# Performance work log

Hardware: AMD Instinct MI355X
Metric: run time of the kernel (lower is better)

## Reference

```python
import jax, jax.numpy as jnp
import numpy as np

B, S, D, H = 4, 2048, 1024, 16
HD = D // H  # 64


def setup_inputs() -> dict:
    key = jax.random.key(0)
    ks = jax.random.split(key, 11)
    scale = 1.0 / np.sqrt(D)
    inp = {
        "query": jax.random.normal(ks[0], (B, S, D), jnp.float32),
        "key": jax.random.normal(ks[1], (B, S, D), jnp.float32),
        "value": jax.random.normal(ks[2], (B, S, D), jnp.float32),
        "mask": jnp.ones((B, 1, 1, S), jnp.float32),
        "wq": jax.random.normal(ks[3], (D, D), jnp.float32) * scale,
        "bq": jnp.zeros((D,), jnp.float32),
        "wk": jax.random.normal(ks[4], (D, D), jnp.float32) * scale,
        "bk": jnp.zeros((D,), jnp.float32),
        "wv": jax.random.normal(ks[5], (D, D), jnp.float32) * scale,
        "bv": jnp.zeros((D,), jnp.float32),
        "wo": jax.random.normal(ks[6], (D, D), jnp.float32) * scale,
        "bo": jnp.zeros((D,), jnp.float32),
    }
    return inp


def reference(query, key, value, mask, wq, bq, wk, bk, wv, bv, wo, bo):
    b = query.shape[0]
    # Dense QKV projections
    q = query @ wq + bq  # [B,S,D]
    k = key @ wk + bk
    v = value @ wv + bv

    def split_heads(x):
        return x.reshape(b, -1, H, HD).transpose(0, 2, 1, 3)  # [B,H,S,HD]

    q, k, v = split_heads(q), split_heads(k), split_heads(v)
    score = jnp.einsum("bhqd,bhkd->bhqk", q, k) / jnp.sqrt(jnp.float32(HD))
    score = score + (1.0 - mask) * -1e9
    alpha = jax.nn.softmax(score, axis=-1)
    context = jnp.einsum("bhqk,bhkd->bhqd", alpha, v)  # [B,H,S,HD]
    context = context.transpose(0, 2, 1, 3).reshape(b, -1, D)
    return context @ wo + bo
```

## Files before the change

### kernel.cpp

```cpp
#include <hip/hip_runtime.h>

using u16 = unsigned short;
using u32 = unsigned int;

typedef float  f32x4  __attribute__((ext_vector_type(4)));
typedef float  f32x16 __attribute__((ext_vector_type(16)));
typedef u32    u32x4  __attribute__((ext_vector_type(4)));
typedef _Float16 f16;
typedef f16 f16x8 __attribute__((ext_vector_type(8)));

#define DEVI static __device__ __forceinline__

constexpr int S_  = 2048;
constexpr int D_  = 1024;
constexpr int HD_ = 64;
constexpr int SH_ = S_*HD_;
constexpr size_t NE_ = 8192ull*1024ull;

DEVI f32x4 mfma16f(f16x8 a, f16x8 b, f32x4 c){
  return __builtin_amdgcn_mfma_f32_16x16x32_f16(a, b, c, 0, 0, 0);
}
DEVI f32x16 mfma32(f16x8 a, f16x8 b, f32x16 c){
  return __builtin_amdgcn_mfma_f32_32x32x16_f16(a, b, c, 0, 0, 0);
}
DEVI float exp2fast(float x){
#if __has_builtin(__builtin_amdgcn_exp2f)
  return __builtin_amdgcn_exp2f(x);
#else
  float r; asm("v_exp_f32 %0, %1" : "=v"(r) : "v"(x)); return r;
#endif
}
DEVI float rcpfast(float x){
#if __has_builtin(__builtin_amdgcn_rcpf)
  return __builtin_amdgcn_rcpf(x);
#else
  float r; asm("v_rcp_f32 %0, %1" : "=v"(r) : "v"(x)); return r;
#endif
}
DEVI u32 pkh(float a, float b){
  return __builtin_bit_cast(u32, __builtin_amdgcn_cvt_pkrtz(a, b));
}
DEVI void gld16(const void* g, void* l){
  __builtin_amdgcn_global_load_lds(
      (const __attribute__((address_space(1))) u32*)g,
      (__attribute__((address_space(3))) u32*)l, 16, 0, 0);
}
DEVI void gld4(const void* g, void* l){
  __builtin_amdgcn_global_load_lds(
      (const __attribute__((address_space(1))) u32*)g,
      (__attribute__((address_space(3))) u32*)l, 4, 0, 0);
}

__global__ __launch_bounds__(256) void wcvt_k(
    const float* __restrict__ wq, const float* __restrict__ wk,
    const float* __restrict__ wv, const float* __restrict__ wo,
    u16* __restrict__ wt)
{
  int z = blockIdx.z;
  const float* W = (z==0)?wq:(z==1)?wk:(z==2)?wv:wo;
  u16* ot = wt + (size_t)z*D_*D_;
  __shared__ float t[64][65];
  int k0 = blockIdx.y*64, n0 = blockIdx.x*64;
  int tid = threadIdx.x;
#pragma unroll
  for (int i=0;i<4;i++){
    int lin = i*256 + tid;
    int r = lin>>4, c = (lin&15)*4;
    f32x4 v = *reinterpret_cast<const f32x4*>(W + (size_t)(k0+r)*D_ + n0 + c);
    t[r][c+0]=v.x; t[r][c+1]=v.y; t[r][c+2]=v.z; t[r][c+3]=v.w;
  }
  __syncthreads();
  int n = tid>>2, c0 = (tid&3)*16;
  alignas(16) u16 hb[16];
#pragma unroll
  for (int i=0;i<16;i++) hb[i] = __builtin_bit_cast(u16, (f16)t[c0+i][n]);
  size_t off = (size_t)(n0+n)*D_ + k0 + c0;
  *reinterpret_cast<u32x4*>(ot+off)   = *reinterpret_cast<u32x4*>(hb);
  *reinterpret_cast<u32x4*>(ot+off+8) = *reinterpret_cast<u32x4*>(hb+8);
}

__global__ __launch_bounds__(256) void madd_k(const float* __restrict__ mask,
                                              float* __restrict__ madd2)
{
  int i = blockIdx.x*256 + threadIdx.x;
  if (i < 4*S_) madd2[i] = (1.0f - mask[i]) * -1442695040.0f;
}

struct GemmArgs {
  const void* A[3];
  const u16*  Wt[3];
  const float* bias[3];
  float*      outF[3];
  u16*        outH[3];
  float       scale[3];
  int         mode[3];
};

template<bool AF32>
__global__ __launch_bounds__(512, 4) void gemm_k(GemmArgs args)
{
  int z = blockIdx.z;
  const float* __restrict__ Af   = (const float*)args.A[z];
  const u16*   __restrict__ Ah   = (const u16*)args.A[z];
  const u16*   __restrict__ Wt   = args.Wt[z];
  const float* __restrict__ bias = args.bias[z];
  int mode = args.mode[z];
  float sc = args.scale[z];

  constexpr int ABYT = 16384;
  constexpr int BUFS = ABYT + 8192;
  __shared__ __align__(16) unsigned char smem[73728];
  char* sbase = (char*)smem;

  int m0 = blockIdx.x*256, n0 = blockIdx.y*128;
  int tid = threadIdx.x, lane = tid&63, w = tid>>6;
  int wm = (w>>1)*64, wn = (w&1)*64;
  int lr = lane&15, lh = lane>>4;

  int offA[2], offB;
#pragma unroll
  for (int j=0;j<2;j++){
    int chunk = w*2 + j;
    int row = chunk*16 + (lane>>2);
    int gs = lane&3;
    offA[j] = row*D_ + (((gs - (row>>1)) & 3)*8);
  }
  {
    int row = w*16 + (lane>>2);
    int gs = lane&3;
    offB = row*D_ + (((gs - (row>>1)) & 3)*8);
  }

  int arow = w*32 + (lane>>1);
  const float* Abase = AF32 ? (Af + (size_t)(m0 + arow)*D_ + (lane&1)*16)
                            : (const float*)nullptr;

  f32x4 acc[4][4];
#pragma unroll
  for (int m=0;m<4;m++)
#pragma unroll
    for (int n=0;n<4;n++) acc[m][n] = f32x4{0.f,0.f,0.f,0.f};

  auto BSTAGE = [&](int kt){
    char* lB = sbase + (kt - (kt/3)*3)*BUFS + ABYT;
    gld16(Wt + (size_t)n0*D_ + kt*32 + offB, lB + w*1024);
  };
  auto ASTAGE16 = [&](int kt){
    char* lA = sbase + (kt - (kt/3)*3)*BUFS;
    const u16* As = Ah + (size_t)m0*D_ + kt*32;
#pragma unroll
    for (int j=0;j<2;j++) gld16(As + offA[j], lA + (w*2+j)*1024);
  };

  f32x4 ra0, ra1, ra2, ra3;

#define AISSUE_M(kt) { \
  ra0 = *reinterpret_cast<const f32x4*>(Abase + (kt)*32 + 0); \
  ra1 = *reinterpret_cast<const f32x4*>(Abase + (kt)*32 + 4); \
  ra2 = *reinterpret_cast<const f32x4*>(Abase + (kt)*32 + 8); \
  ra3 = *reinterpret_cast<const f32x4*>(Abase + (kt)*32 + 12); }

#define CONVERT_M(bufA) { \
  u32x4 w0_, w1_; \
  w0_.x = pkh(ra0.x,ra0.y); w0_.y = pkh(ra0.z,ra0.w); \
  w0_.z = pkh(ra1.x,ra1.y); w0_.w = pkh(ra1.z,ra1.w); \
  w1_.x = pkh(ra2.x,ra2.y); w1_.y = pkh(ra2.z,ra2.w); \
  w1_.z = pkh(ra3.x,ra3.y); w1_.w = pkh(ra3.z,ra3.w); \
  char* dst_ = (bufA) + arow*64; \
  int g0_ = (lane&1)*2; \
  *reinterpret_cast<u32x4*>(dst_ + (((g0_   + (arow>>1))&3)<<4)) = w0_; \
  *reinterpret_cast<u32x4*>(dst_ + (((g0_+1 + (arow>>1))&3)<<4)) = w1_; }

  if constexpr (AF32){
    BSTAGE(0); BSTAGE(1); BSTAGE(2);
    AISSUE_M(0);
    CONVERT_M(sbase);
    AISSUE_M(1);
    asm volatile("s_waitcnt vmcnt(6)" ::: "memory");

    for (int t=0; t<32; ++t){
      int buf = t - (t/3)*3;
      char* bA = sbase + buf*BUFS;
      char* bB = bA + ABYT;

      asm volatile("s_waitcnt lgkmcnt(0)" ::: "memory");
      __builtin_amdgcn_s_barrier();
      __builtin_amdgcn_sched_barrier(0);

      f16x8 af[4], bfr[4];
#pragma unroll
      for (int m=0;m<4;m++){
        int row = wm + m*16 + lr;
        af[m] = *reinterpret_cast<const f16x8*>(bA + row*64 + (((lh + (row>>1)) & 3)<<4));
      }
#pragma unroll
      for (int n=0;n<4;n++){
        int row = wn + n*16 + lr;
        bfr[n] = *reinterpret_cast<const f16x8*>(bB + row*64 + (((lh + (row>>1)) & 3)<<4));
      }
      asm volatile("s_waitcnt lgkmcnt(0)" ::: "memory");
      __builtin_amdgcn_sched_barrier(0);
      __builtin_amdgcn_s_barrier();

      if (t < 31){
        asm volatile("s_waitcnt vmcnt(0)" ::: "memory");
        int nb = (t+1) - ((t+1)/3)*3;
        CONVERT_M(sbase + nb*BUFS);
      }
      if (t < 30) AISSUE_M(t+2);
      if (t < 29) BSTAGE(t+3);

      __builtin_amdgcn_s_setprio(1);
#pragma unroll
      for (int m=0;m<4;m++)
#pragma unroll
        for (int n=0;n<4;n++)
          acc[m][n] = mfma16f(af[m], bfr[n], acc[m][n]);
      __builtin_amdgcn_s_setprio(0);
    }
  } else {
    ASTAGE16(0); BSTAGE(0);
    ASTAGE16(1); BSTAGE(1);
    ASTAGE16(2); BSTAGE(2);

    for (int t=0; t<32; ++t){
      int buf = t - (t/3)*3;
      if (t < 30)       asm volatile("s_waitcnt vmcnt(6)" ::: "memory");
      else if (t == 30) asm volatile("s_waitcnt vmcnt(3)" ::: "memory");
      else              asm volatile("s_waitcnt vmcnt(0)" ::: "memory");
      __builtin_amdgcn_s_barrier();

      char* bA = sbase + buf*BUFS;
      char* bB = bA + ABYT;
      f16x8 af[4], bfr[4];
#pragma unroll
      for (int m=0;m<4;m++){
        int row = wm + m*16 + lr;
        af[m] = *reinterpret_cast<const f16x8*>(bA + row*64 + (((lh + (row>>1)) & 3)<<4));
      }
#pragma unroll
      for (int n=0;n<4;n++){
        int row = wn + n*16 + lr;
        bfr[n] = *reinterpret_cast<const f16x8*>(bB + row*64 + (((lh + (row>>1)) & 3)<<4));
      }
      asm volatile("s_waitcnt lgkmcnt(0)" ::: "memory");
      __builtin_amdgcn_sched_barrier(0);
      __builtin_amdgcn_s_barrier();
      if (t < 29){ ASTAGE16(t+3); BSTAGE(t+3); }

      __builtin_amdgcn_s_setprio(1);
#pragma unroll
      for (int m=0;m<4;m++)
#pragma unroll
        for (int n=0;n<4;n++)
          acc[m][n] = mfma16f(af[m], bfr[n], acc[m][n]);
      __builtin_amdgcn_s_setprio(0);
    }
  }
#undef AISSUE_M
#undef CONVERT_M

  float bsetv[4];
#pragma unroll
  for (int n=0;n<4;n++) bsetv[n] = bias[n0 + wn + n*16 + lr];

  if (mode == 0){
    float* out = args.outF[z];
#pragma unroll
    for (int m=0;m<4;m++)
#pragma unroll
      for (int n=0;n<4;n++)
#pragma unroll
        for (int r=0;r<4;r++){
          int row = m0 + wm + m*16 + lh*4 + r;
          int col = n0 + wn + n*16 + lr;
          out[(size_t)row*D_ + col] = (acc[m][n][r] + bsetv[n])*sc;
        }
  } else if (mode == 1){
    u16* oh = args.outH[z];
#pragma unroll
    for (int m=0;m<4;m++)
#pragma unroll
      for (int n=0;n<4;n++)
#pragma unroll
        for (int r=0;r<4;r++){
          int row = m0 + wm + m*16 + lh*4 + r;
          int col = n0 + wn + n*16 + lr;
          float val = (acc[m][n][r] + bsetv[n])*sc;
          int b = row >> 11, s = row & 2047;
          int hh = col >> 6,  dd = col & 63;
          oh[(size_t)(b*16 + hh)*SH_ + (size_t)s*HD_ + dd] =
              __builtin_bit_cast(u16, (f16)val);
        }
  } else {
    __syncthreads();
    u16* ct = (u16*)sbase;
#pragma unroll
    for (int m=0;m<4;m++)
#pragma unroll
      for (int n=0;n<4;n++)
#pragma unroll
        for (int r=0;r<4;r++){
          int lrow = wm + m*16 + lh*4 + r;
          int lcol = wn + n*16 + lr;
          ct[lrow*132 + lcol] = __builtin_bit_cast(u16, (f16)((acc[m][n][r] + bsetv[n])*sc));
        }
    __syncthreads();
    u16* ovt = args.outH[z];
    int b = m0 >> 11, s0 = m0 & 2047;
    int ch = tid >> 2, quarter = tid & 3;
    int gn = n0 + ch;
    int hh = gn >> 6, dd = gn & 63;
    size_t obase = (size_t)(b*16 + hh)*SH_ + (size_t)dd*S_ + s0 + quarter*64;
#pragma unroll
    for (int i=0;i<8;i++){
      alignas(16) u16 tmp[8];
#pragma unroll
      for (int j=0;j<8;j++) tmp[j] = ct[(quarter*64 + i*8 + j)*132 + ch];
      *reinterpret_cast<u32x4*>(ovt + obase + i*8) = *reinterpret_cast<u32x4*>(tmp);
    }
  }
}

__global__ __launch_bounds__(256, 2) void attn_k(
    const f16* __restrict__ Qf, const f16* __restrict__ Kf,
    const f16* __restrict__ Vt, const float* __restrict__ madd2,
    u16* __restrict__ cf)
{
  constexpr int BUFS = 33280;
  __shared__ __align__(16) unsigned char smem[2*BUFS];
  char* sbase = (char*)smem;

  int flat = blockIdx.x + blockIdx.y*gridDim.x;
  int xcd = flat & 7, ix = flat >> 3;
  int bh = xcd + 8*(ix >> 4);
  int qx = ix & 15;
  int b = bh >> 4, head = bh & 15;

  const f16* Qb = Qf + (size_t)bh*SH_;
  const f16* Kb = Kf + (size_t)bh*SH_;
  const f16* Vb = Vt + (size_t)bh*SH_;
  const float* mb = madd2 + (size_t)b*S_;

  int tid = threadIdx.x, lane = tid&63, w = tid>>6;
  int q31 = lane&31, h = lane>>5;
  int qw = qx*128 + w*32;
  int xorv = (q31&7)<<4;

  f16x8 qb[4];
#pragma unroll
  for (int ks=0;ks<4;ks++)
    qb[ks] = *reinterpret_cast<const f16x8*>(Qb + (size_t)(qw + q31)*HD_ + ks*16 + h*8);

  int offK[4], offV[4];
#pragma unroll
  for (int j=0;j<4;j++){
    int L = (w*4+j)*1024 + lane*16;
    int rK = L>>7;
    int dbyK = (L&127) ^ ((rK&7)<<4);
    offK[j] = rK*HD_ + (dbyK>>1);
    int rV = L>>8;
    int dbyV = (L&255) ^ ((rV&7)<<4);
    offV[j] = rV*S_ + (dbyV>>1);
  }

  u32 one2 = 0x3C003C00u;
  u32x4 onev; onev.x=one2; onev.y=one2; onev.z=one2; onev.w=one2;
  f16x8 vones = __builtin_bit_cast(f16x8, onev);

  f32x16 z16;
#pragma unroll
  for (int r=0;r<16;r++) z16[r] = 0.f;

  f32x16 o[2], ol;
#pragma unroll
  for (int n=0;n<2;n++)
#pragma unroll
    for (int r=0;r<16;r++) o[n][r] = 0.f;
#pragma unroll
  for (int r=0;r<16;r++) ol[r] = 0.f;

  auto STAGE = [&](int buf, int t){
    int kv0 = t*128;
    char* sKb = sbase + buf*BUFS;
    char* sVb = sKb + 16384;
    char* sMb = sKb + 32768;
#pragma unroll
    for (int j=0;j<4;j++)
      gld16(Kb + (size_t)kv0*HD_ + offK[j], sKb + (w*4+j)*1024);
#pragma unroll
    for (int j=0;j<4;j++)
      gld16(Vb + kv0 + offV[j], sVb + (w*4+j)*1024);
    gld4(mb + kv0 + lane, sMb);
    gld4(mb + kv0 + 64 + lane, sMb + 256);
  };

  STAGE(0, 0);
  STAGE(1, 1);

  for (int t=0; t<16; ++t){
    int buf = t&1;
    char* sKb = sbase + buf*BUFS;
    char* sVb = sKb + 16384;
    float* sMb = (float*)(sKb + 32768);

    if (t < 15) asm volatile("s_waitcnt vmcnt(10)" ::: "memory");
    else        asm volatile("s_waitcnt vmcnt(0)"  ::: "memory");
    __builtin_amdgcn_s_barrier();
    __builtin_amdgcn_sched_barrier(0);

    f32x16 stA[2], stB[2];

    __builtin_amdgcn_s_setprio(1);
#pragma unroll
    for (int n=0;n<2;n++){
      int rb = (n*32 + q31)*128;
      f16x8 ka = *reinterpret_cast<const f16x8*>(sKb + ((rb + h*16) ^ xorv));
      stA[n] = mfma32(ka, qb[0], z16);
#pragma unroll
      for (int ks=1;ks<4;ks++){
        ka = *reinterpret_cast<const f16x8*>(sKb + ((rb + ks*32 + h*16) ^ xorv));
        stA[n] = mfma32(ka, qb[ks], stA[n]);
      }
    }
#pragma unroll
    for (int n=0;n<2;n++){
      int rb = (64 + n*32 + q31)*128;
      f16x8 ka = *reinterpret_cast<const f16x8*>(sKb + ((rb + h*16) ^ xorv));
      stB[n] = mfma32(ka, qb[0], z16);
#pragma unroll
      for (int ks=1;ks<4;ks++){
        ka = *reinterpret_cast<const f16x8*>(sKb + ((rb + ks*32 + h*16) ^ xorv));
        stB[n] = mfma32(ka, qb[ks], stB[n]);
      }
    }
    __builtin_amdgcn_s_setprio(0);

    auto SMPV = [&](int sub, f32x16 (&st)[2]){
      float mval = sMb[sub*64 + lane];
      if (__ballot(mval != 0.0f)){
#pragma unroll
        for (int n=0;n<2;n++)
#pragma unroll
          for (int g=0;g<4;g++){
            f32x4 mv = *reinterpret_cast<const f32x4*>(sMb + sub*64 + n*32 + g*8 + h*4);
#pragma unroll
            for (int c=0;c<4;c++) st[n][g*4+c] += mv[c];
          }
      }
#pragma unroll
      for (int n=0;n<2;n++)
#pragma unroll
        for (int r=0;r<16;r++) st[n][r] = exp2fast(st[n][r]);

      f16x8 pa[4];
#pragma unroll
      for (int n=0;n<2;n++){
        u32 x[4], y[4];
#pragma unroll
        for (int T=0;T<4;T++){
          x[T] = pkh(st[n][4*T+0], st[n][4*T+1]);
          y[T] = pkh(st[n][4*T+2], st[n][4*T+3]);
        }
#pragma unroll
        for (int k2=0;k2<2;k2++){
          u32 a0=x[2*k2], b0=x[2*k2+1], a1=y[2*k2], b1=y[2*k2+1];
          asm volatile("v_permlane32_swap_b32 %0, %1" : "+v"(a0), "+v"(b0));
          asm volatile("v_permlane32_swap_b32 %0, %1" : "+v"(a1), "+v"(b1));
          u32x4 wv;
          wv.x = a0;
          wv.y = a1;
          wv.z = b0;
          wv.w = b1;
          pa[2*n+k2] = __builtin_bit_cast(f16x8, wv);
        }
      }

      __builtin_amdgcn_s_setprio(1);
#pragma unroll
      for (int n=0;n<2;n++){
        int rbv = (n*32 + q31)*256 + sub*128;
#pragma unroll
        for (int ks=0;ks<4;ks++){
          f16x8 vbf = *reinterpret_cast<const f16x8*>(sVb + ((rbv + ks*32 + h*16) ^ xorv));
          o[n] = mfma32(pa[ks], vbf, o[n]);
        }
      }
#pragma unroll
      for (int ks=0;ks<4;ks++)
        ol = mfma32(pa[ks], vones, ol);
      __builtin_amdgcn_s_setprio(0);
    };

    SMPV(0, stA);
    SMPV(1, stB);

    asm volatile("s_waitcnt lgkmcnt(0)" ::: "memory");
    __builtin_amdgcn_s_barrier();
    __builtin_amdgcn_sched_barrier(0);
    if (t < 14) STAGE(buf, t+2);
  }

#pragma unroll
  for (int n=0;n<2;n++)
#pragma unroll
    for (int r=0;r<16;r++){
      float inv = rcpfast(ol[r]);
      int s = qw + (r&3) + 8*(r>>2) + 4*h;
      int d = head*HD_ + n*32 + q31;
      cf[((size_t)(b*S_ + s))*D_ + d] = __builtin_bit_cast(u16, (f16)(o[n][r]*inv));
    }
}

extern "C" void kernel_launch(void* const* d_in, const int* in_sizes, int n_in,
                              void* d_out, int out_size, void* d_ws, size_t ws_size,
                              hipStream_t stream)
{
  (void)in_sizes; (void)n_in; (void)out_size;
  const float* query=(const float*)d_in[0];
  const float* key  =(const float*)d_in[1];
  const float* value=(const float*)d_in[2];
  const float* mask =(const float*)d_in[3];
  const float* wq=(const float*)d_in[4];
  const float* bq=(const float*)d_in[5];
  const float* wk=(const float*)d_in[6];
  const float* bk=(const float*)d_in[7];
  const float* wv=(const float*)d_in[8];
  const float* bv=(const float*)d_in[9];
  const float* wo=(const float*)d_in[10];
  const float* bo=(const float*)d_in[11];
  float* out = (float*)d_out;

  const size_t WN = 4ull*1024*1024;
  size_t need = WN*2 + 4*NE_*2 + 8192*4;
  if (ws_size < need) return;

  char* ws = (char*)d_ws;
  u16* wt = (u16*)ws;
  u16* qf = wt + WN;
  u16* kf = qf + NE_;
  u16* vt = kf + NE_;
  u16* cf = vt + NE_;
  float* madd2 = (float*)(cf + NE_);

  const float CSC = 0.18033688011112042f;

  wcvt_k<<<dim3(16,16,4), 256, 0, stream>>>(wq,wk,wv,wo,wt);
  madd_k<<<dim3(32), 256, 0, stream>>>(mask, madd2);

  GemmArgs ga{};
  ga.A[0]=query; ga.A[1]=key; ga.A[2]=value;
  ga.Wt[0]=wt;           ga.Wt[1]=wt+1048576;   ga.Wt[2]=wt+2097152;
  ga.bias[0]=bq; ga.bias[1]=bk; ga.bias[2]=bv;
  ga.scale[0]=CSC; ga.scale[1]=1.0f; ga.scale[2]=1.0f;
  ga.mode[0]=1;  ga.mode[1]=1;  ga.mode[2]=2;
  ga.outH[0]=qf; ga.outH[1]=kf; ga.outH[2]=vt;
  gemm_k<true><<<dim3(32,8,3), 512, 0, stream>>>(ga);

  attn_k<<<dim3(16,64), 256, 0, stream>>>((const f16*)qf,(const f16*)kf,(const f16*)vt,madd2,cf);

  GemmArgs go{};
  go.A[0]=cf;
  go.Wt[0]=wt+3145728;
  go.bias[0]=bo; go.scale[0]=1.0f; go.mode[0]=0; go.outF[0]=out;
  gemm_k<false><<<dim3(32,8,1), 512, 0, stream>>>(go);
}
```

Baseline: 205.0 us.

## Double-buffer fp32 A register prefetch to deepen GEMM load pipeline

```diff
diff --git a/kernel.cpp b/kernel.cpp
--- a/kernel.cpp
+++ b/kernel.cpp
@@ -152,71 +152,86 @@
     for (int j=0;j<2;j++) gld16(As + offA[j], lA + (w*2+j)*1024);
   };
 
-  f32x4 ra0, ra1, ra2, ra3;
-
-#define AISSUE_M(kt) { \
-  ra0 = *reinterpret_cast<const f32x4*>(Abase + (kt)*32 + 0); \
-  ra1 = *reinterpret_cast<const f32x4*>(Abase + (kt)*32 + 4); \
-  ra2 = *reinterpret_cast<const f32x4*>(Abase + (kt)*32 + 8); \
-  ra3 = *reinterpret_cast<const f32x4*>(Abase + (kt)*32 + 12); }
-
-#define CONVERT_M(bufA) { \
+  f32x4 s0a, s0b, s0c, s0d;
+  f32x4 s1a, s1b, s1c, s1d;
+
+#define AISSUE0(kt) { \
+  s0a = *reinterpret_cast<const f32x4*>(Abase + (kt)*32 + 0); \
+  s0b = *reinterpret_cast<const f32x4*>(Abase + (kt)*32 + 4); \
+  s0c = *reinterpret_cast<const f32x4*>(Abase + (kt)*32 + 8); \
+  s0d = *reinterpret_cast<const f32x4*>(Abase + (kt)*32 + 12); }
+#define AISSUE1(kt) { \
+  s1a = *reinterpret_cast<const f32x4*>(Abase + (kt)*32 + 0); \
+  s1b = *reinterpret_cast<const f32x4*>(Abase + (kt)*32 + 4); \
+  s1c = *reinterpret_cast<const f32x4*>(Abase + (kt)*32 + 8); \
+  s1d = *reinterpret_cast<const f32x4*>(Abase + (kt)*32 + 12); }
+
+#define CONVERT_GEN(pa,pb,pc,pd,bufA) { \
   u32x4 w0_, w1_; \
-  w0_.x = pkh(ra0.x,ra0.y); w0_.y = pkh(ra0.z,ra0.w); \
-  w0_.z = pkh(ra1.x,ra1.y); w0_.w = pkh(ra1.z,ra1.w); \
-  w1_.x = pkh(ra2.x,ra2.y); w1_.y = pkh(ra2.z,ra2.w); \
-  w1_.z = pkh(ra3.x,ra3.y); w1_.w = pkh(ra3.z,ra3.w); \
+  w0_.x = pkh(pa.x,pa.y); w0_.y = pkh(pa.z,pa.w); \
+  w0_.z = pkh(pb.x,pb.y); w0_.w = pkh(pb.z,pb.w); \
+  w1_.x = pkh(pc.x,pc.y); w1_.y = pkh(pc.z,pc.w); \
+  w1_.z = pkh(pd.x,pd.y); w1_.w = pkh(pd.z,pd.w); \
   char* dst_ = (bufA) + arow*64; \
   int g0_ = (lane&1)*2; \
   *reinterpret_cast<u32x4*>(dst_ + (((g0_   + (arow>>1))&3)<<4)) = w0_; \
   *reinterpret_cast<u32x4*>(dst_ + (((g0_+1 + (arow>>1))&3)<<4)) = w1_; }
+#define CONVERT0(bufA) CONVERT_GEN(s0a,s0b,s0c,s0d,bufA)
+#define CONVERT1(bufA) CONVERT_GEN(s1a,s1b,s1c,s1d,bufA)
+
+#define AF32_BODY(t, CVTSET) { \
+  int buf_ = (t) - ((t)/3)*3; \
+  char* bA_ = sbase + buf_*BUFS; \
+  char* bB_ = bA_ + ABYT; \
+  if ((t) < 30)      asm volatile("s_waitcnt vmcnt(10)" ::: "memory"); \
+  else if ((t)==30)  asm volatile("s_waitcnt vmcnt(5)"  ::: "memory"); \
+  else               asm volatile("s_waitcnt vmcnt(0)"  ::: "memory"); \
+  asm volatile("s_waitcnt lgkmcnt(0)" ::: "memory"); \
+  __builtin_amdgcn_s_barrier(); \
+  __builtin_amdgcn_sched_barrier(0); \
+  f16x8 af_[4], bf_[4]; \
+  _Pragma("unroll") \
+  for (int m=0;m<4;m++){ \
+    int row = wm + m*16 + lr; \
+    af_[m] = *reinterpret_cast<const f16x8*>(bA_ + row*64 + (((lh + (row>>1)) & 3)<<4)); \
+  } \
+  _Pragma("unroll") \
+  for (int n=0;n<4;n++){ \
+    int row = wn + n*16 + lr; \
+    bf_[n] = *reinterpret_cast<const f16x8*>(bB_ + row*64 + (((lh + (row>>1)) & 3)<<4)); \
+  } \
+  asm volatile("s_waitcnt lgkmcnt(0)" ::: "memory"); \
+  __builtin_amdgcn_sched_barrier(0); \
+  __builtin_amdgcn_s_barrier(); \
+  if ((t) < 31){ \
+    int nb_ = ((t)+1) - (((t)+1)/3)*3; \
+    if constexpr (CVTSET == 0) { CONVERT0(sbase + nb_*BUFS); } \
+    else                       { CONVERT1(sbase + nb_*BUFS); } \
+  } \
+  if ((t) < 29){ \
+    if constexpr (CVTSET == 0) { AISSUE0((t)+3); } \
+    else                       { AISSUE1((t)+3); } \
+    BSTAGE((t)+3); \
+  } \
+  __builtin_amdgcn_s_setprio(1); \
+  _Pragma("unroll") \
+  for (int m=0;m<4;m++) \
+    _Pragma("unroll") \
+    for (int n=0;n<4;n++) \
+      acc[m][n] = mfma16f(af_[m], bf_[n], acc[m][n]); \
+  __builtin_amdgcn_s_setprio(0); }
 
   if constexpr (AF32){
     BSTAGE(0); BSTAGE(1); BSTAGE(2);
-    AISSUE_M(0);
-    CONVERT_M(sbase);
-    AISSUE_M(1);
-    asm volatile("s_waitcnt vmcnt(6)" ::: "memory");
-
-    for (int t=0; t<32; ++t){
-      int buf = t - (t/3)*3;
-      char* bA = sbase + buf*BUFS;
-      char* bB = bA + ABYT;
-
-      asm volatile("s_waitcnt lgkmcnt(0)" ::: "memory");
-      __builtin_amdgcn_s_barrier();
-      __builtin_amdgcn_sched_barrier(0);
-
-      f16x8 af[4], bfr[4];
-#pragma unroll
-      for (int m=0;m<4;m++){
-        int row = wm + m*16 + lr;
-        af[m] = *reinterpret_cast<const f16x8*>(bA + row*64 + (((lh + (row>>1)) & 3)<<4));
-      }
-#pragma unroll
-      for (int n=0;n<4;n++){
-        int row = wn + n*16 + lr;
-        bfr[n] = *reinterpret_cast<const f16x8*>(bB + row*64 + (((lh + (row>>1)) & 3)<<4));
-      }
-      asm volatile("s_waitcnt lgkmcnt(0)" ::: "memory");
-      __builtin_amdgcn_sched_barrier(0);
-      __builtin_amdgcn_s_barrier();
-
-      if (t < 31){
-        asm volatile("s_waitcnt vmcnt(0)" ::: "memory");
-        int nb = (t+1) - ((t+1)/3)*3;
-        CONVERT_M(sbase + nb*BUFS);
-      }
-      if (t < 30) AISSUE_M(t+2);
-      if (t < 29) BSTAGE(t+3);
-
-      __builtin_amdgcn_s_setprio(1);
-#pragma unroll
-      for (int m=0;m<4;m++)
-#pragma unroll
-        for (int n=0;n<4;n++)
-          acc[m][n] = mfma16f(af[m], bfr[n], acc[m][n]);
-      __builtin_amdgcn_s_setprio(0);
+    AISSUE0(0);
+    CONVERT0(sbase);
+    AISSUE1(1);
+    AISSUE0(2);
+
+    for (int i=0; i<16; ++i){
+      int u = 2*i, v = 2*i + 1;
+      AF32_BODY(u, 1);
+      AF32_BODY(v, 0);
     }
   } else {
     ASTAGE16(0); BSTAGE(0);
@@ -257,8 +272,12 @@
       __builtin_amdgcn_s_setprio(0);
     }
   }
-#undef AISSUE_M
-#undef CONVERT_M
+#undef AF32_BODY
+#undef CONVERT0
+#undef CONVERT1
+#undef CONVERT_GEN
+#undef AISSUE0
+#undef AISSUE1
 
   float bsetv[4];
 #pragma unroll
```

New measurement: 492.0 us. +140.0%, slower.
